# Kernel optimization log

Hardware: AMD Instinct MI355X
Metric: run time of the kernel (lower is better)

The kernel has to match this reference:

```python
import jax, jax.numpy as jnp
import numpy as np

N = 100000   # nodes
E = 1600000  # directed edges (avg degree 16)
IN = 256     # input feature dim


def _gcn_norm(src, dst, n):
    # PyG gcn_norm with unit edge weights: deg computed on destination,
    # norm = deg^{-1/2}[src] * deg^{-1/2}[dst]
    deg = jax.ops.segment_sum(jnp.ones_like(dst, jnp.float32), dst, num_segments=n)
    dinv = jnp.where(deg > 0, jax.lax.rsqrt(deg), 0.0)
    return dinv[src] * dinv[dst]


def _gcn_conv(x, W, b, src, dst, norm, n):
    h = x @ W                          # [N, out] dense transform first (PyG order)
    msg = norm[:, None] * h[src]       # gather + scale  [E+N, out]
    agg = jax.ops.segment_sum(msg, dst, num_segments=n)  # scatter-add
    return agg + b


def setup_inputs() -> dict:
    key = jax.random.key(0)
    ks = jax.random.split(key, 5)
    x = jax.random.normal(ks[0], (N, IN), jnp.float32)
    edge_index = jax.random.randint(ks[1], (2, E), 0, N, dtype=jnp.int32)
    W1 = jax.random.normal(ks[2], (IN, 64), jnp.float32) * (1.0 / np.sqrt(IN))
    b1 = jnp.zeros((64,), jnp.float32)
    W2 = jax.random.normal(ks[3], (64, 32), jnp.float32) * (1.0 / np.sqrt(64))
    b2 = jnp.zeros((32,), jnp.float32)
    Wlin = jax.random.normal(ks[4], (32, 1), jnp.float32) * (1.0 / np.sqrt(32))
    blin = jnp.zeros((1,), jnp.float32)
    return {"x": x, "edge_index": edge_index, "W1": W1, "b1": b1,
            "W2": W2, "b2": b2, "Wlin": Wlin, "blin": blin}


def reference(x, edge_index, W1, b1, W2, b2, Wlin, blin):
    n = x.shape[0]
    loops = jnp.arange(n, dtype=edge_index.dtype)  # add self-loops (GCNConv default)
    src = jnp.concatenate([edge_index[0], loops])
    dst = jnp.concatenate([edge_index[1], loops])
    norm = _gcn_norm(src, dst, n)                  # same for both layers
    h = jax.nn.relu(_gcn_conv(x, W1, b1, src, dst, norm, n))
    h = jax.nn.relu(_gcn_conv(h, W2, b2, src, dst, norm, n))
    return h @ Wlin + blin
```

## Files before the change

### kernel.cpp

```cpp
#include <hip/hip_runtime.h>
#include <hip/hip_fp16.h>
#include <math.h>


#define BSH  9
#define BCAP 12288

typedef _Float16 half8 __attribute__((ext_vector_type(8)));
typedef _Float16 half4 __attribute__((ext_vector_type(4)));
typedef float floatx4 __attribute__((ext_vector_type(4)));

static __global__ __launch_bounds__(256) void k_wfrag(const float* __restrict__ W1,
                                                      _Float16* __restrict__ w1f,
                                                      int* __restrict__ bkt_cnt) {
    int t = threadIdx.x;
    bkt_cnt[t] = 0;
    for (int idx = t; idx < 2048; idx += 256) {
        int kb = idx >> 8;
        int nt = (idx >> 6) & 3;
        int l  = idx & 63;
        int k0 = kb * 32 + ((l >> 4) << 3);
        int nn = nt * 16 + (l & 15);
        half8 b;
        #pragma unroll
        for (int j = 0; j < 8; ++j) b[j] = (_Float16)W1[(k0 + j) * 64 + nn];
        *(half8*)(w1f + (size_t)idx * 8) = b;
    }
}

static __global__ __launch_bounds__(256) void k_fat(const float* __restrict__ x,
                                                    const _Float16* __restrict__ w1f,
                                                    _Float16* __restrict__ h1f,
                                                    const int* __restrict__ src,
                                                    const int* __restrict__ dst,
                                                    int* __restrict__ bkt_cnt,
                                                    int* __restrict__ epack,
                                                    int n, int e, int nScat) {
    __shared__ alignas(16) char smem[25600];
    int t = threadIdx.x;

    if ((int)blockIdx.x < nScat) {
        int*           sp    = (int*)smem;
        unsigned char* sbkt  = (unsigned char*)(smem + 16384);
        int*           cnt   = (int*)(smem + 20480);
        int*           loff  = (int*)(smem + 21504);
        int*           lcur  = (int*)(smem + 22528);
        int*           gbase = (int*)(smem + 23552);
        int*           sh    = (int*)(smem + 24576);
        int cb = blockIdx.x * 4096;
        int cc = min(4096, e - cb);

        cnt[t] = 0;
        __syncthreads();
        int ep[16]; unsigned char eb[16];
        int nv = 0;
        #pragma unroll
        for (int k = 0; k < 16; ++k) {
            int i = cb + k * 256 + t;
            if (i < e) {
                int s = src[i], d = dst[i];
                int b = d >> BSH;
                ep[nv] = ((d & 511) << 17) | s;
                eb[nv] = (unsigned char)b;
                atomicAdd(&cnt[b], 1);
                ++nv;
            }
        }
        __syncthreads();
        int v = cnt[t];
        sh[t] = v;
        __syncthreads();
        for (int o = 1; o < 256; o <<= 1) {
            int u = (t >= o) ? sh[t - o] : 0;
            __syncthreads();
            sh[t] += u;
            __syncthreads();
        }
        loff[t] = sh[t] - v;
        lcur[t] = sh[t] - v;
        if (v > 0) gbase[t] = t * BCAP + atomicAdd(&bkt_cnt[t], v);
        __syncthreads();
        for (int k = 0; k < nv; ++k) {
            int b = eb[k];
            int p = atomicAdd(&lcur[b], 1);
            sp[p] = ep[k];
            sbkt[p] = (unsigned char)b;
        }
        __syncthreads();
        for (int i = t; i < cc; i += 256) {
            int b = sbkt[i];
            epack[gbase[b] + (i - loff[b])] = sp[i];
        }
    } else {
        int l = t & 63;
        int w = t >> 6;
        int r0 = (blockIdx.x - nScat) * 128;

        const float* sg[2];
        #pragma unroll
        for (int mt = 0; mt < 2; ++mt) {
            int gr = r0 + w * 32 + mt * 16 + (l >> 2);
            gr = gr < n ? gr : n - 1;
            sg[mt] = x + (size_t)gr * 256 + (l & 3) * 8;
        }
        int sidx = (l & 15) * 4 + (l >> 4);

        floatx4 acc[2][4];
        #pragma unroll
        for (int mt = 0; mt < 2; ++mt)
            #pragma unroll
            for (int nt = 0; nt < 4; ++nt)
                acc[mt][nt] = (floatx4){0.f, 0.f, 0.f, 0.f};

        #pragma unroll
        for (int kb = 0; kb < 8; ++kb) {
            float4 stA[2][2];
            #pragma unroll
            for (int mt = 0; mt < 2; ++mt) {
                stA[mt][0] = *(const float4*)(sg[mt] + kb * 32);
                stA[mt][1] = *(const float4*)(sg[mt] + kb * 32 + 4);
            }
            half8 a[2];
            #pragma unroll
            for (int mt = 0; mt < 2; ++mt) {
                #pragma unroll
                for (int j = 0; j < 2; ++j) {
                    float f0 = __shfl(stA[mt][j].x, sidx);
                    float f1 = __shfl(stA[mt][j].y, sidx);
                    float f2 = __shfl(stA[mt][j].z, sidx);
                    float f3 = __shfl(stA[mt][j].w, sidx);
                    a[mt][j * 4 + 0] = (_Float16)f0;
                    a[mt][j * 4 + 1] = (_Float16)f1;
                    a[mt][j * 4 + 2] = (_Float16)f2;
                    a[mt][j * 4 + 3] = (_Float16)f3;
                }
            }
            #pragma unroll
            for (int nt = 0; nt < 4; ++nt) {
                half8 b = *(const half8*)(w1f + ((size_t)(kb * 4 + nt) * 64 + l) * 8);
                acc[0][nt] = __builtin_amdgcn_mfma_f32_16x16x32_f16(a[0], b, acc[0][nt], 0, 0, 0);
                acc[1][nt] = __builtin_amdgcn_mfma_f32_16x16x32_f16(a[1], b, acc[1][nt], 0, 0, 0);
            }
        }

        int quad = l >> 4;
        int col  = l & 15;
        int rb0  = r0 + w * 32;
        #pragma unroll
        for (int mt = 0; mt < 2; ++mt) {
            #pragma unroll
            for (int r = 0; r < 4; ++r) {
                int rr = rb0 + mt * 16 + quad * 4 + r;
                if (rr < n) {
                    _Float16* o = h1f + (size_t)rr * 64 + col;
                    #pragma unroll
                    for (int nt = 0; nt < 4; ++nt)
                        o[nt * 16] = (_Float16)acc[mt][nt][r];
                }
            }
        }
    }
}

static __global__ __launch_bounds__(512) void k_bfinal(const int* __restrict__ bkt_cnt,
                                                       const int* __restrict__ epack,
                                                       float* __restrict__ dinv,
                                                       int* __restrict__ offs,
                                                       int* __restrict__ csr_src, int n) {
    __shared__ int cnt[512], sh[512], lcur[512];
    int t = threadIdx.x;
    int base = blockIdx.x << BSH;
    int e0 = blockIdx.x * BCAP;
    int e1 = e0 + bkt_cnt[blockIdx.x];
    cnt[t] = 0;
    __syncthreads();
    for (int i = e0 + t; i < e1; i += 512) atomicAdd(&cnt[epack[i] >> 17], 1);
    __syncthreads();
    int v = cnt[t];
    if (base + t < n) dinv[base + t] = 1.0f / sqrtf((float)(v + 1));
    sh[t] = v;
    __syncthreads();
    for (int o = 1; o < 512; o <<= 1) {
        int u = (t >= o) ? sh[t - o] : 0;
        __syncthreads();
        sh[t] += u;
        __syncthreads();
    }
    int incl = sh[t];
    if (base + t < n) offs[base + t] = e0 + incl;
    lcur[t] = e0 + incl - v;
    __syncthreads();
    for (int i = e0 + t; i < e1; i += 512) {
        int p = epack[i];
        int d = p >> 17;
        int pos = atomicAdd(&lcur[d], 1);
        csr_src[pos] = p & 0x1FFFF;
    }
}

static __global__ __launch_bounds__(512) void k_wpack(int* __restrict__ csr_src,
                                                      const float* __restrict__ dinv,
                                                      const int* __restrict__ bkt_cnt) {
    int b  = blockIdx.x;
    int e0 = b * BCAP;
    int e1 = e0 + bkt_cnt[b];
    for (int i = e0 + threadIdx.x; i < e1; i += 512) {
        int s = csr_src[i];
        int q = (int)(dinv[s] * 32767.0f + 0.5f);
        csr_src[i] = s | (q << 17);
    }
}

static __global__ __launch_bounds__(256) void k_agg1gemm2(const int* __restrict__ offs,
                                                          const int* __restrict__ csr_src,
                                                          const float* __restrict__ dinv,
                                                          const uint2* __restrict__ h1q,
                                                          const float* __restrict__ b1,
                                                          const float* __restrict__ W2,
                                                          __half2* __restrict__ h2h, int n) {
    __shared__ float Wl[64 * 32];
    __shared__ float aggL[16][64];
    int t = threadIdx.x;
    *(float4*)(Wl + t * 4)        = *(const float4*)(W2 + t * 4);
    *(float4*)(Wl + t * 4 + 1024) = *(const float4*)(W2 + t * 4 + 1024);

    int li = t & 15;
    int ni = t >> 4;
    int node  = blockIdx.x * 16 + ni;
    int nodeC = node < n ? node : n - 1;
    int start = (nodeC & 511) ? offs[nodeC - 1] : (nodeC >> BSH) * BCAP;
    int end   = offs[nodeC];
    float dd  = dinv[nodeC];

    uint2 su = h1q[(size_t)nodeC * 16 + li];
    float2 s01 = __half22float2(*(const __half2*)&su.x);
    float2 s23 = __half22float2(*(const __half2*)&su.y);
    float a0 = dd * s01.x, a1 = dd * s01.y, a2 = dd * s23.x, a3 = dd * s23.y;

    const float QS = 1.0f / 32767.0f;
    int j = start;
    for (; j + 7 < end; j += 8) {
        int pk[8];
        #pragma unroll
        for (int u = 0; u < 8; ++u) pk[u] = csr_src[j + u];
        uint2 vv[8]; float wq[8];
        #pragma unroll
        for (int u = 0; u < 8; ++u) {
            int s = pk[u] & 0x1FFFF;
            wq[u] = (float)(((unsigned)pk[u]) >> 17) * QS;
            vv[u] = h1q[(size_t)s * 16 + li];
        }
        #pragma unroll
        for (int u = 0; u < 8; ++u) {
            float2 v01 = __half22float2(*(const __half2*)&vv[u].x);
            float2 v23 = __half22float2(*(const __half2*)&vv[u].y);
            a0 += wq[u] * v01.x; a1 += wq[u] * v01.y;
            a2 += wq[u] * v23.x; a3 += wq[u] * v23.y;
        }
    }
    for (; j < end; ++j) {
        int p = csr_src[j];
        int s = p & 0x1FFFF;
        float wv = (float)(((unsigned)p) >> 17) * QS;
        uint2 v = h1q[(size_t)s * 16 + li];
        float2 v01 = __half22float2(*(const __half2*)&v.x);
        float2 v23 = __half22float2(*(const __half2*)&v.y);
        a0 += wv * v01.x; a1 += wv * v01.y;
        a2 += wv * v23.x; a3 += wv * v23.y;
    }
    float4 bb = *(const float4*)(b1 + li * 4);
    aggL[ni][li * 4 + 0] = fmaxf(dd * a0 + bb.x, 0.f);
    aggL[ni][li * 4 + 1] = fmaxf(dd * a1 + bb.y, 0.f);
    aggL[ni][li * 4 + 2] = fmaxf(dd * a2 + bb.z, 0.f);
    aggL[ni][li * 4 + 3] = fmaxf(dd * a3 + bb.w, 0.f);
    __syncthreads();

    if (node < n) {
        float s0 = 0.f, s1 = 0.f;
        #pragma unroll
        for (int k = 0; k < 64; ++k) {
            float a = aggL[ni][k];
            float2 wv = *(const float2*)(Wl + k * 32 + li * 2);
            s0 += a * wv.x;
            s1 += a * wv.y;
        }
        h2h[(size_t)node * 16 + li] = __float22half2_rn(make_float2(s0, s1));
    }
}

static __global__ __launch_bounds__(256) void k_gather2f(const int* __restrict__ offs,
                                                         const int* __restrict__ csr_src,
                                                         const float* __restrict__ dinv,
                                                         const uint2* __restrict__ h2q,
                                                         const float* __restrict__ b2,
                                                         const float* __restrict__ Wlin,
                                                         const float* __restrict__ blin,
                                                         float* __restrict__ out, int n) {
    int g    = blockIdx.x * 256 + threadIdx.x;
    int node = g >> 3;
    if (node >= n) return;
    int li = g & 7;
    int start = (node & 511) ? offs[node - 1] : (node >> BSH) * BCAP;
    int end   = offs[node];
    float dd  = dinv[node];

    uint2 su = h2q[(size_t)node * 8 + li];
    float2 s01 = __half22float2(*(const __half2*)&su.x);
    float2 s23 = __half22float2(*(const __half2*)&su.y);
    float a0 = dd * s01.x, a1 = dd * s01.y, a2 = dd * s23.x, a3 = dd * s23.y;

    const float QS = 1.0f / 32767.0f;
    int j = start;
    for (; j + 7 < end; j += 8) {
        int pk[8];
        #pragma unroll
        for (int u = 0; u < 8; ++u) pk[u] = csr_src[j + u];
        uint2 vv[8]; float wq[8];
        #pragma unroll
        for (int u = 0; u < 8; ++u) {
            int s = pk[u] & 0x1FFFF;
            wq[u] = (float)(((unsigned)pk[u]) >> 17) * QS;
            vv[u] = h2q[(size_t)s * 8 + li];
        }
        #pragma unroll
        for (int u = 0; u < 8; ++u) {
            float2 v01 = __half22float2(*(const __half2*)&vv[u].x);
            float2 v23 = __half22float2(*(const __half2*)&vv[u].y);
            a0 += wq[u] * v01.x; a1 += wq[u] * v01.y;
            a2 += wq[u] * v23.x; a3 += wq[u] * v23.y;
        }
    }
    for (; j < end; ++j) {
        int p = csr_src[j];
        int s = p & 0x1FFFF;
        float wv = (float)(((unsigned)p) >> 17) * QS;
        uint2 v = h2q[(size_t)s * 8 + li];
        float2 v01 = __half22float2(*(const __half2*)&v.x);
        float2 v23 = __half22float2(*(const __half2*)&v.y);
        a0 += wv * v01.x; a1 += wv * v01.y;
        a2 += wv * v23.x; a3 += wv * v23.y;
    }
    float4 bb = *(const float4*)(b2 + li * 4);
    float4 wl = *(const float4*)(Wlin + li * 4);
    float val = fmaxf(dd * a0 + bb.x, 0.f) * wl.x +
                fmaxf(dd * a1 + bb.y, 0.f) * wl.y +
                fmaxf(dd * a2 + bb.z, 0.f) * wl.z +
                fmaxf(dd * a3 + bb.w, 0.f) * wl.w;
    val += __shfl_xor(val, 4);
    val += __shfl_xor(val, 2);
    val += __shfl_xor(val, 1);
    if (li == 0) out[node] = val + blin[0];
}

extern "C" void kernel_launch(void* const* d_in, const int* in_sizes, int n_in,
                              void* d_out, int out_size, void* d_ws, size_t ws_size,
                              hipStream_t stream) {
    const float* x    = (const float*)d_in[0];
    const int*   ei   = (const int*)d_in[1];
    const float* W1   = (const float*)d_in[2];
    const float* b1   = (const float*)d_in[3];
    const float* W2   = (const float*)d_in[4];
    const float* b2   = (const float*)d_in[5];
    const float* Wlin = (const float*)d_in[6];
    const float* blin = (const float*)d_in[7];
    float* out = (float*)d_out;

    const int n = in_sizes[0] / 256;
    const int e = in_sizes[1] / 2;
    const int* src = ei;
    const int* dst = ei + e;
    const int nbkt  = (n + (1 << BSH) - 1) >> BSH;
    const int nScat = (e + 4095) / 4096;
    const int nGemm = (n + 127) / 128;

    char* wp = (char*)d_ws;
    _Float16* h1f = (_Float16*)wp;
    uint2*    h1q = (uint2*)wp;       wp += (size_t)n * 32 * 4;
    __half2*  h2h = (__half2*)wp;
    uint2*    h2q = (uint2*)wp;       wp += (size_t)n * 32 * 2;
    float*    dinv = (float*)wp;      wp += (size_t)n * 4;
    int*      offs = (int*)wp;        wp += (size_t)n * 4;
    int*      csr_src = (int*)wp;     wp += (size_t)nbkt * BCAP * 4;
    int*      epack = (int*)wp;       wp += (size_t)nbkt * BCAP * 4;
    int*      bkt_cnt = (int*)wp;     wp += 256 * 4;
    _Float16* w1f = (_Float16*)wp;

    dim3 B(256);
    k_wfrag <<<1, B, 0, stream>>>(W1, w1f, bkt_cnt);
    k_fat   <<<nScat + nGemm, B, 0, stream>>>(x, w1f, h1f, src, dst, bkt_cnt, epack, n, e, nScat);
    k_bfinal<<<nbkt, 512, 0, stream>>>(bkt_cnt, epack, dinv, offs, csr_src, n);
    k_wpack <<<nbkt, 512, 0, stream>>>(csr_src, dinv, bkt_cnt);
    k_agg1gemm2<<<(n + 15) / 16, B, 0, stream>>>(offs, csr_src, dinv, h1q, b1, W2, h2h, n);
    k_gather2f <<<(n * 8 + 255) / 256, B, 0, stream>>>(offs, csr_src, dinv, h2q,
                                                       b2, Wlin, blin, out, n);
}
```

Baseline: 286.9 us.

## Split fused scatter/GEMM kernel and prefetch x loads in GEMM1

The fused kernel that ran edge bucketing and the first dense transform in different blocks is split into two separate launches, k_gemm1 and k_scat. The GEMM now prefetches four k-blocks of x ahead in registers, using an asm barrier to keep the loads early. It also converts to fp16 before the lane shuffle, which halves the number of shuffles. This raises memory-level parallelism in the bandwidth-bound x read, at the cost of more registers, one extra launch, and losing the overlap between scatter and GEMM blocks.

```diff
diff --git a/kernel.cpp b/kernel.cpp
--- a/kernel.cpp
+++ b/kernel.cpp
@@ -28,135 +28,154 @@
     }
 }
 
-static __global__ __launch_bounds__(256) void k_fat(const float* __restrict__ x,
-                                                    const _Float16* __restrict__ w1f,
-                                                    _Float16* __restrict__ h1f,
-                                                    const int* __restrict__ src,
-                                                    const int* __restrict__ dst,
-                                                    int* __restrict__ bkt_cnt,
-                                                    int* __restrict__ epack,
-                                                    int n, int e, int nScat) {
+static __global__ __launch_bounds__(256) void k_scat(const int* __restrict__ src,
+                                                     const int* __restrict__ dst,
+                                                     int* __restrict__ bkt_cnt,
+                                                     int* __restrict__ epack,
+                                                     int e) {
     __shared__ alignas(16) char smem[25600];
     int t = threadIdx.x;
-
-    if ((int)blockIdx.x < nScat) {
-        int*           sp    = (int*)smem;
-        unsigned char* sbkt  = (unsigned char*)(smem + 16384);
-        int*           cnt   = (int*)(smem + 20480);
-        int*           loff  = (int*)(smem + 21504);
-        int*           lcur  = (int*)(smem + 22528);
-        int*           gbase = (int*)(smem + 23552);
-        int*           sh    = (int*)(smem + 24576);
-        int cb = blockIdx.x * 4096;
-        int cc = min(4096, e - cb);
-
-        cnt[t] = 0;
+    int*           sp    = (int*)smem;
+    unsigned char* sbkt  = (unsigned char*)(smem + 16384);
+    int*           cnt   = (int*)(smem + 20480);
+    int*           loff  = (int*)(smem + 21504);
+    int*           lcur  = (int*)(smem + 22528);
+    int*           gbase = (int*)(smem + 23552);
+    int*           sh    = (int*)(smem + 24576);
+    int cb = blockIdx.x * 4096;
+    int cc = min(4096, e - cb);
+
+    cnt[t] = 0;
+    __syncthreads();
+    int ep[16]; unsigned char eb[16];
+    int nv = 0;
+    #pragma unroll
+    for (int k = 0; k < 16; ++k) {
+        int i = cb + k * 256 + t;
+        if (i < e) {
+            int s = src[i], d = dst[i];
+            int b = d >> BSH;
+            ep[nv] = ((d & 511) << 17) | s;
+            eb[nv] = (unsigned char)b;
+            atomicAdd(&cnt[b], 1);
+            ++nv;
+        }
+    }
+    __syncthreads();
+    int v = cnt[t];
+    sh[t] = v;
+    __syncthreads();
+    for (int o = 1; o < 256; o <<= 1) {
+        int u = (t >= o) ? sh[t - o] : 0;
         __syncthreads();
-        int ep[16]; unsigned char eb[16];
-        int nv = 0;
-        #pragma unroll
-        for (int k = 0; k < 16; ++k) {
-            int i = cb + k * 256 + t;
-            if (i < e) {
-                int s = src[i], d = dst[i];
-                int b = d >> BSH;
-                ep[nv] = ((d & 511) << 17) | s;
-                eb[nv] = (unsigned char)b;
-                atomicAdd(&cnt[b], 1);
-                ++nv;
-            }
-        }
+        sh[t] += u;
         __syncthreads();
-        int v = cnt[t];
-        sh[t] = v;
-        __syncthreads();
-        for (int o = 1; o < 256; o <<= 1) {
-            int u = (t >= o) ? sh[t - o] : 0;
-            __syncthreads();
-            sh[t] += u;
-            __syncthreads();
-        }
-        loff[t] = sh[t] - v;
-        lcur[t] = sh[t] - v;
-        if (v > 0) gbase[t] = t * BCAP + atomicAdd(&bkt_cnt[t], v);
-        __syncthreads();
-        for (int k = 0; k < nv; ++k) {
-            int b = eb[k];
-            int p = atomicAdd(&lcur[b], 1);
-            sp[p] = ep[k];
-            sbkt[p] = (unsigned char)b;
-        }
-        __syncthreads();
-        for (int i = t; i < cc; i += 256) {
-            int b = sbkt[i];
-            epack[gbase[b] + (i - loff[b])] = sp[i];
-        }
-    } else {
-        int l = t & 63;
-        int w = t >> 6;
-        int r0 = (blockIdx.x - nScat) * 128;
-
-        const float* sg[2];
+    }
+    loff[t] = sh[t] - v;
+    lcur[t] = sh[t] - v;
+    if (v > 0) gbase[t] = t * BCAP + atomicAdd(&bkt_cnt[t], v);
+    __syncthreads();
+    for (int k = 0; k < nv; ++k) {
+        int b = eb[k];
+        int p = atomicAdd(&lcur[b], 1);
+        sp[p] = ep[k];
+        sbkt[p] = (unsigned char)b;
+    }
+    __syncthreads();
+    for (int i = t; i < cc; i += 256) {
+        int b = sbkt[i];
+        epack[gbase[b] + (i - loff[b])] = sp[i];
+    }
+}
+
+static __global__ __launch_bounds__(256) void k_gemm1(const float* __restrict__ x,
+                                                      const _Float16* __restrict__ w1f,
+                                                      _Float16* __restrict__ h1f,
+                                                      int n) {
+    int t = threadIdx.x;
+    int l = t & 63;
+    int w = t >> 6;
+    int r0 = blockIdx.x * 128;
+
+    const float* sg[2];
+    #pragma unroll
+    for (int mt = 0; mt < 2; ++mt) {
+        int gr = r0 + w * 32 + mt * 16 + (l >> 2);
+        gr = gr < n ? gr : n - 1;
+        sg[mt] = x + (size_t)gr * 256 + (l & 3) * 8;
+    }
+    int sidx = (l & 15) * 4 + (l >> 4);
+
+    floatx4 acc[2][4];
+    #pragma unroll
+    for (int mt = 0; mt < 2; ++mt)
+        #pragma unroll
+        for (int nt = 0; nt < 4; ++nt)
+            acc[mt][nt] = (floatx4){0.f, 0.f, 0.f, 0.f};
+
+    float4 st[8][2][2];
+    #pragma unroll
+    for (int kb = 0; kb < 4; ++kb)
         #pragma unroll
         for (int mt = 0; mt < 2; ++mt) {
-            int gr = r0 + w * 32 + mt * 16 + (l >> 2);
-            gr = gr < n ? gr : n - 1;
-            sg[mt] = x + (size_t)gr * 256 + (l & 3) * 8;
-        }
-        int sidx = (l & 15) * 4 + (l >> 4);
-
-        floatx4 acc[2][4];
-        #pragma unroll
-        for (int mt = 0; mt < 2; ++mt)
-            #pragma unroll
-            for (int nt = 0; nt < 4; ++nt)
-                acc[mt][nt] = (floatx4){0.f, 0.f, 0.f, 0.f};
-
-        #pragma unroll
-        for (int kb = 0; kb < 8; ++kb) {
-            float4 stA[2][2];
+            st[kb][mt][0] = *(const float4*)(sg[mt] + kb * 32);
+            st[kb][mt][1] = *(const float4*)(sg[mt] + kb * 32 + 4);
+        }
+
+    #pragma unroll
+    for (int kb = 0; kb < 8; ++kb) {
+        if (kb + 4 < 8) {
             #pragma unroll
             for (int mt = 0; mt < 2; ++mt) {
-                stA[mt][0] = *(const float4*)(sg[mt] + kb * 32);
-                stA[mt][1] = *(const float4*)(sg[mt] + kb * 32 + 4);
+                st[kb + 4][mt][0] = *(const float4*)(sg[mt] + (kb + 4) * 32);
+                st[kb + 4][mt][1] = *(const float4*)(sg[mt] + (kb + 4) * 32 + 4);
             }
-            half8 a[2];
-            #pragma unroll
-            for (int mt = 0; mt < 2; ++mt) {
+        }
+        asm volatile("" :: "v"(st[kb][0][0].x), "v"(st[kb][0][0].y),
+                           "v"(st[kb][0][0].z), "v"(st[kb][0][0].w),
+                           "v"(st[kb][0][1].x), "v"(st[kb][0][1].y),
+                           "v"(st[kb][0][1].z), "v"(st[kb][0][1].w),
+                           "v"(st[kb][1][0].x), "v"(st[kb][1][0].y),
+                           "v"(st[kb][1][0].z), "v"(st[kb][1][0].w),
+                           "v"(st[kb][1][1].x), "v"(st[kb][1][1].y),
+                           "v"(st[kb][1][1].z), "v"(st[kb][1][1].w) : "memory");
+        half8 a[2];
+        #pragma unroll
+        for (int mt = 0; mt < 2; ++mt) {
+            half4 lo = {(_Float16)st[kb][mt][0].x, (_Float16)st[kb][mt][0].y,
+                        (_Float16)st[kb][mt][0].z, (_Float16)st[kb][mt][0].w};
+            half4 hi = {(_Float16)st[kb][mt][1].x, (_Float16)st[kb][mt][1].y,
+                        (_Float16)st[kb][mt][1].z, (_Float16)st[kb][mt][1].w};
+            int2 wlo = __builtin_bit_cast(int2, lo);
+            int2 whi = __builtin_bit_cast(int2, hi);
+            int r0w = __shfl(wlo.x, sidx);
+            int r1w = __shfl(wlo.y, sidx);
+            int r2w = __shfl(whi.x, sidx);
+            int r3w = __shfl(whi.y, sidx);
+            int4 rr = {r0w, r1w, r2w, r3w};
+            a[mt] = __builtin_bit_cast(half8, rr);
+        }
+        #pragma unroll
+        for (int nt = 0; nt < 4; ++nt) {
+            half8 b = *(const half8*)(w1f + ((size_t)(kb * 4 + nt) * 64 + l) * 8);
+            acc[0][nt] = __builtin_amdgcn_mfma_f32_16x16x32_f16(a[0], b, acc[0][nt], 0, 0, 0);
+            acc[1][nt] = __builtin_amdgcn_mfma_f32_16x16x32_f16(a[1], b, acc[1][nt], 0, 0, 0);
+        }
+    }
+
+    int quad = l >> 4;
+    int col  = l & 15;
+    int rb0  = r0 + w * 32;
+    #pragma unroll
+    for (int mt = 0; mt < 2; ++mt) {
+        #pragma unroll
+        for (int r = 0; r < 4; ++r) {
+            int rr = rb0 + mt * 16 + quad * 4 + r;
+            if (rr < n) {
+                _Float16* o = h1f + (size_t)rr * 64 + col;
                 #pragma unroll
-                for (int j = 0; j < 2; ++j) {
-                    float f0 = __shfl(stA[mt][j].x, sidx);
-                    float f1 = __shfl(stA[mt][j].y, sidx);
-                    float f2 = __shfl(stA[mt][j].z, sidx);
-                    float f3 = __shfl(stA[mt][j].w, sidx);
-                    a[mt][j * 4 + 0] = (_Float16)f0;
-                    a[mt][j * 4 + 1] = (_Float16)f1;
-                    a[mt][j * 4 + 2] = (_Float16)f2;
-                    a[mt][j * 4 + 3] = (_Float16)f3;
-                }
-            }
-            #pragma unroll
-            for (int nt = 0; nt < 4; ++nt) {
-                half8 b = *(const half8*)(w1f + ((size_t)(kb * 4 + nt) * 64 + l) * 8);
-                acc[0][nt] = __builtin_amdgcn_mfma_f32_16x16x32_f16(a[0], b, acc[0][nt], 0, 0, 0);
-                acc[1][nt] = __builtin_amdgcn_mfma_f32_16x16x32_f16(a[1], b, acc[1][nt], 0, 0, 0);
-            }
-        }
-
-        int quad = l >> 4;
-        int col  = l & 15;
-        int rb0  = r0 + w * 32;
-        #pragma unroll
-        for (int mt = 0; mt < 2; ++mt) {
-            #pragma unroll
-            for (int r = 0; r < 4; ++r) {
-                int rr = rb0 + mt * 16 + quad * 4 + r;
-                if (rr < n) {
-                    _Float16* o = h1f + (size_t)rr * 64 + col;
-                    #pragma unroll
-                    for (int nt = 0; nt < 4; ++nt)
-                        o[nt * 16] = (_Float16)acc[mt][nt][r];
-                }
+                for (int nt = 0; nt < 4; ++nt)
+                    o[nt * 16] = (_Float16)acc[mt][nt][r];
             }
         }
     }
@@ -387,7 +406,8 @@
 
     dim3 B(256);
     k_wfrag <<<1, B, 0, stream>>>(W1, w1f, bkt_cnt);
-    k_fat   <<<nScat + nGemm, B, 0, stream>>>(x, w1f, h1f, src, dst, bkt_cnt, epack, n, e, nScat);
+    k_gemm1 <<<nGemm, B, 0, stream>>>(x, w1f, h1f, n);
+    k_scat  <<<nScat, B, 0, stream>>>(src, dst, bkt_cnt, epack, e);
     k_bfinal<<<nbkt, 512, 0, stream>>>(bkt_cnt, epack, dinv, offs, csr_src, n);
     k_wpack <<<nbkt, 512, 0, stream>>>(csr_src, dinv, bkt_cnt);
     k_agg1gemm2<<<(n + 15) / 16, B, 0, stream>>>(offs, csr_src, dinv, h1q, b1, W2, h2h, n);
```

New measurement: 307.2 us. +7.1%, slower.

## Drop packed-weight pass and widen gather lanes to 16-byte loads

Applied to the files above, without the earlier changes.

Removes the k_wpack kernel that quantized dinv into the upper bits of csr_src. The aggregation kernels now load dinv[src] directly per edge. Each lane gathers 8 halves with a uint4 load instead of 4 halves with a uint2, which halves the lanes per node and doubles the nodes per block. This saves one launch and a full pass over the edge array, and it issues fewer, wider gather transactions. In exchange it adds an extra random 4-byte dinv load per edge and raises per-thread register use.

```diff
diff --git a/kernel.cpp b/kernel.cpp
--- a/kernel.cpp
+++ b/kernel.cpp
@@ -198,155 +198,168 @@
     }
 }
 
-static __global__ __launch_bounds__(512) void k_wpack(int* __restrict__ csr_src,
-                                                      const float* __restrict__ dinv,
-                                                      const int* __restrict__ bkt_cnt) {
-    int b  = blockIdx.x;
-    int e0 = b * BCAP;
-    int e1 = e0 + bkt_cnt[b];
-    for (int i = e0 + threadIdx.x; i < e1; i += 512) {
-        int s = csr_src[i];
-        int q = (int)(dinv[s] * 32767.0f + 0.5f);
-        csr_src[i] = s | (q << 17);
-    }
-}
-
 static __global__ __launch_bounds__(256) void k_agg1gemm2(const int* __restrict__ offs,
                                                           const int* __restrict__ csr_src,
                                                           const float* __restrict__ dinv,
-                                                          const uint2* __restrict__ h1q,
+                                                          const uint4* __restrict__ h1q,
                                                           const float* __restrict__ b1,
                                                           const float* __restrict__ W2,
                                                           __half2* __restrict__ h2h, int n) {
     __shared__ float Wl[64 * 32];
-    __shared__ float aggL[16][64];
+    __shared__ float aggL[32][65];
     int t = threadIdx.x;
     *(float4*)(Wl + t * 4)        = *(const float4*)(W2 + t * 4);
     *(float4*)(Wl + t * 4 + 1024) = *(const float4*)(W2 + t * 4 + 1024);
 
-    int li = t & 15;
-    int ni = t >> 4;
-    int node  = blockIdx.x * 16 + ni;
+    int li = t & 7;
+    int ni = t >> 3;
+    int node  = blockIdx.x * 32 + ni;
     int nodeC = node < n ? node : n - 1;
     int start = (nodeC & 511) ? offs[nodeC - 1] : (nodeC >> BSH) * BCAP;
     int end   = offs[nodeC];
     float dd  = dinv[nodeC];
 
-    uint2 su = h1q[(size_t)nodeC * 16 + li];
-    float2 s01 = __half22float2(*(const __half2*)&su.x);
-    float2 s23 = __half22float2(*(const __half2*)&su.y);
-    float a0 = dd * s01.x, a1 = dd * s01.y, a2 = dd * s23.x, a3 = dd * s23.y;
-
-    const float QS = 1.0f / 32767.0f;
+    float a[8];
+    {
+        uint4 su = h1q[(size_t)nodeC * 8 + li];
+        const __half2* hp = (const __half2*)&su;
+        #pragma unroll
+        for (int q = 0; q < 4; ++q) {
+            float2 f = __half22float2(hp[q]);
+            a[2 * q] = dd * f.x; a[2 * q + 1] = dd * f.y;
+        }
+    }
+
     int j = start;
     for (; j + 7 < end; j += 8) {
-        int pk[8];
-        #pragma unroll
-        for (int u = 0; u < 8; ++u) pk[u] = csr_src[j + u];
-        uint2 vv[8]; float wq[8];
+        int sk[8];
+        #pragma unroll
+        for (int u = 0; u < 8; ++u) sk[u] = csr_src[j + u];
+        float wq[8]; uint4 vv[8];
         #pragma unroll
         for (int u = 0; u < 8; ++u) {
-            int s = pk[u] & 0x1FFFF;
-            wq[u] = (float)(((unsigned)pk[u]) >> 17) * QS;
-            vv[u] = h1q[(size_t)s * 16 + li];
+            wq[u] = dinv[sk[u]];
+            vv[u] = h1q[(size_t)sk[u] * 8 + li];
         }
         #pragma unroll
         for (int u = 0; u < 8; ++u) {
-            float2 v01 = __half22float2(*(const __half2*)&vv[u].x);
-            float2 v23 = __half22float2(*(const __half2*)&vv[u].y);
-            a0 += wq[u] * v01.x; a1 += wq[u] * v01.y;
-            a2 += wq[u] * v23.x; a3 += wq[u] * v23.y;
+            const __half2* hp = (const __half2*)&vv[u];
+            #pragma unroll
+            for (int q = 0; q < 4; ++q) {
+                float2 f = __half22float2(hp[q]);
+                a[2 * q] += wq[u] * f.x; a[2 * q + 1] += wq[u] * f.y;
+            }
         }
     }
     for (; j < end; ++j) {
-        int p = csr_src[j];
-        int s = p & 0x1FFFF;
-        float wv = (float)(((unsigned)p) >> 17) * QS;
-        uint2 v = h1q[(size_t)s * 16 + li];
-        float2 v01 = __half22float2(*(const __half2*)&v.x);
-        float2 v23 = __half22float2(*(const __half2*)&v.y);
-        a0 += wv * v01.x; a1 += wv * v01.y;
-        a2 += wv * v23.x; a3 += wv * v23.y;
-    }
-    float4 bb = *(const float4*)(b1 + li * 4);
-    aggL[ni][li * 4 + 0] = fmaxf(dd * a0 + bb.x, 0.f);
-    aggL[ni][li * 4 + 1] = fmaxf(dd * a1 + bb.y, 0.f);
-    aggL[ni][li * 4 + 2] = fmaxf(dd * a2 + bb.z, 0.f);
-    aggL[ni][li * 4 + 3] = fmaxf(dd * a3 + bb.w, 0.f);
+        int s = csr_src[j];
+        float wv = dinv[s];
+        uint4 v = h1q[(size_t)s * 8 + li];
+        const __half2* hp = (const __half2*)&v;
+        #pragma unroll
+        for (int q = 0; q < 4; ++q) {
+            float2 f = __half22float2(hp[q]);
+            a[2 * q] += wv * f.x; a[2 * q + 1] += wv * f.y;
+        }
+    }
+
+    float4 bb0 = *(const float4*)(b1 + li * 8);
+    float4 bb1 = *(const float4*)(b1 + li * 8 + 4);
+    aggL[ni][li * 8 + 0] = fmaxf(dd * a[0] + bb0.x, 0.f);
+    aggL[ni][li * 8 + 1] = fmaxf(dd * a[1] + bb0.y, 0.f);
+    aggL[ni][li * 8 + 2] = fmaxf(dd * a[2] + bb0.z, 0.f);
+    aggL[ni][li * 8 + 3] = fmaxf(dd * a[3] + bb0.w, 0.f);
+    aggL[ni][li * 8 + 4] = fmaxf(dd * a[4] + bb1.x, 0.f);
+    aggL[ni][li * 8 + 5] = fmaxf(dd * a[5] + bb1.y, 0.f);
+    aggL[ni][li * 8 + 6] = fmaxf(dd * a[6] + bb1.z, 0.f);
+    aggL[ni][li * 8 + 7] = fmaxf(dd * a[7] + bb1.w, 0.f);
     __syncthreads();
 
     if (node < n) {
-        float s0 = 0.f, s1 = 0.f;
+        float s0 = 0.f, s1 = 0.f, s2 = 0.f, s3 = 0.f;
         #pragma unroll
         for (int k = 0; k < 64; ++k) {
-            float a = aggL[ni][k];
-            float2 wv = *(const float2*)(Wl + k * 32 + li * 2);
-            s0 += a * wv.x;
-            s1 += a * wv.y;
-        }
-        h2h[(size_t)node * 16 + li] = __float22half2_rn(make_float2(s0, s1));
+            float av = aggL[ni][k];
+            float4 wv = *(const float4*)(Wl + k * 32 + li * 4);
+            s0 += av * wv.x; s1 += av * wv.y; s2 += av * wv.z; s3 += av * wv.w;
+        }
+        h2h[(size_t)node * 16 + li * 2]     = __float22half2_rn(make_float2(s0, s1));
+        h2h[(size_t)node * 16 + li * 2 + 1] = __float22half2_rn(make_float2(s2, s3));
     }
 }
 
 static __global__ __launch_bounds__(256) void k_gather2f(const int* __restrict__ offs,
                                                          const int* __restrict__ csr_src,
                                                          const float* __restrict__ dinv,
-                                                         const uint2* __restrict__ h2q,
+                                                         const uint4* __restrict__ h2q,
                                                          const float* __restrict__ b2,
                                                          const float* __restrict__ Wlin,
                                                          const float* __restrict__ blin,
                                                          float* __restrict__ out, int n) {
     int g    = blockIdx.x * 256 + threadIdx.x;
-    int node = g >> 3;
+    int node = g >> 2;
     if (node >= n) return;
-    int li = g & 7;
+    int li = g & 3;
     int start = (node & 511) ? offs[node - 1] : (node >> BSH) * BCAP;
     int end   = offs[node];
     float dd  = dinv[node];
 
-    uint2 su = h2q[(size_t)node * 8 + li];
-    float2 s01 = __half22float2(*(const __half2*)&su.x);
-    float2 s23 = __half22float2(*(const __half2*)&su.y);
-    float a0 = dd * s01.x, a1 = dd * s01.y, a2 = dd * s23.x, a3 = dd * s23.y;
-
-    const float QS = 1.0f / 32767.0f;
+    float a[8];
+    {
+        uint4 su = h2q[(size_t)node * 4 + li];
+        const __half2* hp = (const __half2*)&su;
+        #pragma unroll
+        for (int q = 0; q < 4; ++q) {
+            float2 f = __half22float2(hp[q]);
+            a[2 * q] = dd * f.x; a[2 * q + 1] = dd * f.y;
+        }
+    }
+
     int j = start;
     for (; j + 7 < end; j += 8) {
-        int pk[8];
-        #pragma unroll
-        for (int u = 0; u < 8; ++u) pk[u] = csr_src[j + u];
-        uint2 vv[8]; float wq[8];
+        int sk[8];
+        #pragma unroll
+        for (int u = 0; u < 8; ++u) sk[u] = csr_src[j + u];
+        float wq[8]; uint4 vv[8];
         #pragma unroll
         for (int u = 0; u < 8; ++u) {
-            int s = pk[u] & 0x1FFFF;
-            wq[u] = (float)(((unsigned)pk[u]) >> 17) * QS;
-            vv[u] = h2q[(size_t)s * 8 + li];
+            wq[u] = dinv[sk[u]];
+            vv[u] = h2q[(size_t)sk[u] * 4 + li];
         }
         #pragma unroll
         for (int u = 0; u < 8; ++u) {
-            float2 v01 = __half22float2(*(const __half2*)&vv[u].x);
-            float2 v23 = __half22float2(*(const __half2*)&vv[u].y);
-            a0 += wq[u] * v01.x; a1 += wq[u] * v01.y;
-            a2 += wq[u] * v23.x; a3 += wq[u] * v23.y;
+            const __half2* hp = (const __half2*)&vv[u];
+            #pragma unroll
+            for (int q = 0; q < 4; ++q) {
+                float2 f = __half22float2(hp[q]);
+                a[2 * q] += wq[u] * f.x; a[2 * q + 1] += wq[u] * f.y;
+            }
         }
     }
     for (; j < end; ++j) {
-        int p = csr_src[j];
-        int s = p & 0x1FFFF;
-        float wv = (float)(((unsigned)p) >> 17) * QS;
-        uint2 v = h2q[(size_t)s * 8 + li];
-        float2 v01 = __half22float2(*(const __half2*)&v.x);
-        float2 v23 = __half22float2(*(const __half2*)&v.y);
-        a0 += wv * v01.x; a1 += wv * v01.y;
-        a2 += wv * v23.x; a3 += wv * v23.y;
-    }
-    float4 bb = *(const float4*)(b2 + li * 4);
-    float4 wl = *(const float4*)(Wlin + li * 4);
-    float val = fmaxf(dd * a0 + bb.x, 0.f) * wl.x +
-                fmaxf(dd * a1 + bb.y, 0.f) * wl.y +
-                fmaxf(dd * a2 + bb.z, 0.f) * wl.z +
-                fmaxf(dd * a3 + bb.w, 0.f) * wl.w;
-    val += __shfl_xor(val, 4);
+        int s = csr_src[j];
+        float wv = dinv[s];
+        uint4 v = h2q[(size_t)s * 4 + li];
+        const __half2* hp = (const __half2*)&v;
+        #pragma unroll
+        for (int q = 0; q < 4; ++q) {
+            float2 f = __half22float2(hp[q]);
+            a[2 * q] += wv * f.x; a[2 * q + 1] += wv * f.y;
+        }
+    }
+
+    float4 bb0 = *(const float4*)(b2 + li * 8);
+    float4 bb1 = *(const float4*)(b2 + li * 8 + 4);
+    float4 wl0 = *(const float4*)(Wlin + li * 8);
+    float4 wl1 = *(const float4*)(Wlin + li * 8 + 4);
+    float val = fmaxf(dd * a[0] + bb0.x, 0.f) * wl0.x +
+                fmaxf(dd * a[1] + bb0.y, 0.f) * wl0.y +
+                fmaxf(dd * a[2] + bb0.z, 0.f) * wl0.z +
+                fmaxf(dd * a[3] + bb0.w, 0.f) * wl0.w +
+                fmaxf(dd * a[4] + bb1.x, 0.f) * wl1.x +
+                fmaxf(dd * a[5] + bb1.y, 0.f) * wl1.y +
+                fmaxf(dd * a[6] + bb1.z, 0.f) * wl1.z +
+                fmaxf(dd * a[7] + bb1.w, 0.f) * wl1.w;
     val += __shfl_xor(val, 2);
     val += __shfl_xor(val, 1);
     if (li == 0) out[node] = val + blin[0];
@@ -375,9 +388,9 @@
 
     char* wp = (char*)d_ws;
     _Float16* h1f = (_Float16*)wp;
-    uint2*    h1q = (uint2*)wp;       wp += (size_t)n * 32 * 4;
+    uint4*    h1q = (uint4*)wp;       wp += (size_t)n * 32 * 4;
     __half2*  h2h = (__half2*)wp;
-    uint2*    h2q = (uint2*)wp;       wp += (size_t)n * 32 * 2;
+    uint4*    h2q = (uint4*)wp;       wp += (size_t)n * 32 * 2;
     float*    dinv = (float*)wp;      wp += (size_t)n * 4;
     int*      offs = (int*)wp;        wp += (size_t)n * 4;
     int*      csr_src = (int*)wp;     wp += (size_t)nbkt * BCAP * 4;
@@ -389,8 +402,7 @@
     k_wfrag <<<1, B, 0, stream>>>(W1, w1f, bkt_cnt);
     k_fat   <<<nScat + nGemm, B, 0, stream>>>(x, w1f, h1f, src, dst, bkt_cnt, epack, n, e, nScat);
     k_bfinal<<<nbkt, 512, 0, stream>>>(bkt_cnt, epack, dinv, offs, csr_src, n);
-    k_wpack <<<nbkt, 512, 0, stream>>>(csr_src, dinv, bkt_cnt);
-    k_agg1gemm2<<<(n + 15) / 16, B, 0, stream>>>(offs, csr_src, dinv, h1q, b1, W2, h2h, n);
-    k_gather2f <<<(n * 8 + 255) / 256, B, 0, stream>>>(offs, csr_src, dinv, h2q,
+    k_agg1gemm2<<<(n + 31) / 32, B, 0, stream>>>(offs, csr_src, dinv, h1q, b1, W2, h2h, n);
+    k_gather2f <<<(n * 4 + 255) / 256, B, 0, stream>>>(offs, csr_src, dinv, h2q,
                                                        b2, Wlin, blin, out, n);
 }
```

Measured after the change: 286.7 us. No clear change (-0.1%).
